# Kernel tuning notes

Hardware: AMD Instinct MI355X
Metric: run time of the kernel (lower is better)

Reference implementation:

```python
import jax, jax.numpy as jnp
import numpy as np
from jax import lax

B = 16384
N_NUM = 32
N_CAT = 16
D = 256
D_HID = 512
N_LAYERS = 8
VOCAB = 100001  # total_cats + 1
OUT_DIM = 2
TOT_FEAT = N_NUM + N_CAT
EPS = 1e-5


def _layernorm(x, g, b):
    mu = jnp.mean(x, axis=-1, keepdims=True)
    var = jnp.mean(jnp.square(x - mu), axis=-1, keepdims=True)
    return (x - mu) * lax.rsqrt(var + EPS) * g + b


def setup_inputs() -> dict:
    key = jax.random.key(0)
    ks = jax.random.split(key, 16)
    s = 0.02
    return {
        "x_numerical": jax.random.normal(ks[0], (B, N_NUM, 1), dtype=jnp.float32),
        "x_categorical_idx": jax.random.randint(ks[1], (B, N_CAT), 0, VOCAB - 1, dtype=jnp.int32),
        # per-feature Linear(1, D): weight [N_NUM, D], bias [N_NUM, D]
        "w_num": jax.random.normal(ks[2], (N_NUM, D), dtype=jnp.float32) * s,
        "b_num": jnp.zeros((N_NUM, D), dtype=jnp.float32),
        "cat_embed": jax.random.normal(ks[3], (VOCAB, D), dtype=jnp.float32) * s,
        "W_first": jax.random.normal(ks[4], (TOT_FEAT * D, D), dtype=jnp.float32) * s,
        "b_first": jnp.zeros((D,), dtype=jnp.float32),
        # stacked block params, leading dim = N_LAYERS
        "ln_g": jnp.ones((N_LAYERS, D), dtype=jnp.float32),
        "ln_b": jnp.zeros((N_LAYERS, D), dtype=jnp.float32),
        "W1s": jax.random.normal(ks[5], (N_LAYERS, D, D_HID), dtype=jnp.float32) * s,
        "b1s": jnp.zeros((N_LAYERS, D_HID), dtype=jnp.float32),
        "W2s": jax.random.normal(ks[6], (N_LAYERS, D_HID, D), dtype=jnp.float32) * s,
        "b2s": jnp.zeros((N_LAYERS, D), dtype=jnp.float32),
        "g_f": jnp.ones((D,), dtype=jnp.float32),
        "beta_f": jnp.zeros((D,), dtype=jnp.float32),
        "W_head": jax.random.normal(ks[7], (D, OUT_DIM), dtype=jnp.float32) * s,
        "b_head": jnp.zeros((OUT_DIM,), dtype=jnp.float32),
    }


def reference(x_numerical, x_categorical_idx, w_num, b_num, cat_embed,
              W_first, b_first, ln_g, ln_b, W1s, b1s, W2s, b2s,
              g_f, beta_f, W_head, b_head):
    # numerical embeddings: per-feature Linear(1, D), vectorized over features
    x_val = x_numerical[:, :, 0:1]                       # [B, N_NUM, 1]
    x_n_emb = x_val * w_num[None] + b_num[None]          # [B, N_NUM, D]
    x_c_emb = cat_embed[x_categorical_idx]               # [B, N_CAT, D]
    x = jnp.concatenate([x_n_emb, x_c_emb], axis=1)      # [B, TOT_FEAT, D]
    x = x.reshape(x.shape[0], -1)                        # [B, TOT_FEAT*D]
    x = x @ W_first + b_first                            # [B, D]

    def block(h, params):
        g, bn, W1, b1, W2, b2 = params
        out = _layernorm(h, g, bn)
        out = jax.nn.relu(out @ W1 + b1)                 # dropout = identity (eval)
        out = out @ W2 + b2
        return h + out, None

    x, _ = lax.scan(block, x, (ln_g, ln_b, W1s, b1s, W2s, b2s))
    x = _layernorm(x, g_f, beta_f)
    logits = x @ W_head + b_head                         # [B, OUT_DIM]
    return logits
```

## Files before the change

### kernel.cpp

```cpp
#include <hip/hip_runtime.h>

typedef unsigned short u16;
typedef unsigned int u32;
typedef __attribute__((ext_vector_type(8))) short bf16x8;
typedef __attribute__((ext_vector_type(4))) float f32x4;

#define LDK 72

__device__ __forceinline__ u16 f2bf(float f) {
    u32 u = __float_as_uint(f);
    u += 0x7fffu + ((u >> 16) & 1u);
    return (u16)(u >> 16);
}

__device__ __forceinline__ f32x4 mfma16(bf16x8 a, bf16x8 b, f32x4 c) {
    return __builtin_amdgcn_mfma_f32_16x16x32_bf16(a, b, c, 0, 0, 0);
}


__global__ __launch_bounds__(256) void prep_u_kernel(
    const float* __restrict__ w_num, const float* __restrict__ b_num,
    const float* __restrict__ W_first, float* __restrict__ U, float* __restrict__ P)
{
    __shared__ float wrow[256];
    __shared__ float brow[256];
    int j = threadIdx.x, f = blockIdx.x;
    wrow[j] = w_num[f * 256 + j];
    brow[j] = b_num[f * 256 + j];
    __syncthreads();
    float au = 0.f, ap = 0.f;
#pragma unroll 8
    for (int k = 0; k < 256; k++) {
        float w = W_first[(size_t)((f << 8) + k) * 256 + j];
        au = fmaf(wrow[k], w, au);
        ap = fmaf(brow[k], w, ap);
    }
    U[f * 256 + j] = au;
    P[f * 256 + j] = ap;
}

__global__ __launch_bounds__(256) void prep_c0_kernel(
    const float* __restrict__ b_first, const float* __restrict__ P, float* __restrict__ c0)
{
    int j = threadIdx.x;
    float a = b_first[j];
#pragma unroll 8
    for (int f = 0; f < 32; f++) a += P[f * 256 + j];
    c0[j] = a;
}

__global__ __launch_bounds__(256) void transpose_kernel(
    const float* __restrict__ in, u16* __restrict__ out,
    int R, int C, int ldo, int k_off, size_t in_stride, size_t out_stride)
{
    __shared__ float t[64][65];
    in  += (size_t)blockIdx.z * in_stride;
    out += (size_t)blockIdx.z * out_stride;
    const int tid = threadIdx.x;
    const int r0 = blockIdx.x * 64, c0 = blockIdx.y * 64;
#pragma unroll
    for (int i = 0; i < 16; i++) {
        int e = tid + i * 256;
        int r = e >> 6, c = e & 63;
        float v = (r0 + r < R) ? in[(size_t)(r0 + r) * C + c0 + c] : 0.f;
        t[c][r] = v;
    }
    __syncthreads();
#pragma unroll
    for (int i = 0; i < 2; i++) {
        int e = tid + i * 256;
        int c = e >> 3, r8 = (e & 7) * 8;
        u16 tmp[8];
#pragma unroll
        for (int x = 0; x < 8; x++) tmp[x] = f2bf(t[c][r8 + x]);
        *(bf16x8*)&out[(size_t)(c0 + c) * ldo + k_off + r0 + r8] = *(bf16x8*)tmp;
    }
}

#define FBM 64

#define GATHER(KQ, G0, G1)                                                    \
    {                                                                         \
        int chunk = tid;                                                      \
        int r = chunk >> 4, c4 = chunk & 15;                                  \
        int k = (KQ) + c4 * 4;                                                \
        int rowi = (k < 4096) ? sidx[r * 16 + ((k >> 8) & 15)] : 0;           \
        G0 = *(const float4*)&cemb[(size_t)rowi * 256 + (k & 255)];           \
        if (k >= 4096) {                                                      \
            if (k < 4128) {                                                   \
                int c = r * 32 + (k - 4096);                                  \
                G0.x = sx[c]; G0.y = sx[c + 1];                               \
                G0.z = sx[c + 2]; G0.w = sx[c + 3];                           \
            } else G0 = make_float4(0.f, 0.f, 0.f, 0.f);                      \
        }                                                                     \
        chunk = tid + 512;                                                    \
        r = chunk >> 4; c4 = chunk & 15;                                      \
        k = (KQ) + c4 * 4;                                                    \
        rowi = (k < 4096) ? sidx[r * 16 + ((k >> 8) & 15)] : 0;               \
        G1 = *(const float4*)&cemb[(size_t)rowi * 256 + (k & 255)];           \
        if (k >= 4096) {                                                      \
            if (k < 4128) {                                                   \
                int c = r * 32 + (k - 4096);                                  \
                G1.x = sx[c]; G1.y = sx[c + 1];                               \
                G1.z = sx[c + 2]; G1.w = sx[c + 3];                           \
            } else G1 = make_float4(0.f, 0.f, 0.f, 0.f);                      \
        }                                                                     \
    }

#define WRITE_A(BUF, G0, G1)                                                  \
    {                                                                         \
        int chunk = tid;                                                      \
        int r = chunk >> 4, c4 = chunk & 15;                                  \
        ushort4 o;                                                            \
        o.x = f2bf(G0.x); o.y = f2bf(G0.y); o.z = f2bf(G0.z); o.w = f2bf(G0.w); \
        *(ushort4*)&Ab[BUF][r * LDK + c4 * 4] = o;                            \
        chunk = tid + 512;                                                    \
        r = chunk >> 4; c4 = chunk & 15;                                      \
        o.x = f2bf(G1.x); o.y = f2bf(G1.y); o.z = f2bf(G1.z); o.w = f2bf(G1.w); \
        *(ushort4*)&Ab[BUF][r * LDK + c4 * 4] = o;                            \
    }

#define DMA_B(BUF, KQ)                                                        \
    _Pragma("unroll")                                                         \
    for (int it = 0; it < 4; it++) {                                          \
        int chunk = it * 512 + tid;                                           \
        int r = chunk >> 3;                                                   \
        int c8 = (chunk & 7) ^ (r & 7);                                       \
        const u16* src = &BT[(size_t)r * 4160 + (KQ) + c8 * 8];               \
        __builtin_amdgcn_global_load_lds(                                     \
            (const __attribute__((address_space(1))) void*)src,               \
            (__attribute__((address_space(3))) void*)&Bb[BUF][(it * 512 + wv * 64) * 8], \
            16, 0, 0);                                                        \
    }

#define COMPUTE(AB, BB)                                                       \
    _Pragma("unroll")                                                         \
    for (int kk = 0; kk < 64; kk += 32) {                                     \
        bf16x8 af[2], bfr[4];                                                 \
        _Pragma("unroll")                                                     \
        for (int i = 0; i < 2; i++)                                           \
            af[i] = *(const bf16x8*)&Ab[AB][(wm * 32 + i * 16 + l16) * LDK + kk + quad * 8]; \
        _Pragma("unroll")                                                     \
        for (int j = 0; j < 4; j++) {                                         \
            int row = wn * 64 + j * 16 + l16;                                 \
            int c8L = quad + (kk >> 3);                                       \
            bfr[j] = *(const bf16x8*)&Bb[BB][row * 64 + ((c8L ^ (row & 7)) * 8)]; \
        }                                                                     \
        _Pragma("unroll")                                                     \
        for (int i = 0; i < 2; i++)                                           \
            _Pragma("unroll")                                                 \
            for (int j = 0; j < 4; j++)                                       \
                acc[i][j] = mfma16(af[i], bfr[j], acc[i][j]);                 \
    }

#define ITER(S, KQ, G0, G1)                                                   \
    {                                                                         \
        WRITE_A((S + 1) & 1, G0, G1);                                         \
        int kq2 = (KQ) + 128; if (kq2 > 4096) kq2 = 4096;                     \
        DMA_B((S + 2) & 3, kq2);                                              \
        __builtin_amdgcn_sched_barrier(0);                                    \
        GATHER((KQ) + 192, G0, G1);                                           \
        __builtin_amdgcn_sched_barrier(0);                                    \
        COMPUTE(S & 1, S);                                                    \
        asm volatile("s_waitcnt vmcnt(8) lgkmcnt(0)" ::: "memory");           \
        __builtin_amdgcn_s_barrier();                                         \
        __builtin_amdgcn_sched_barrier(0);                                    \
    }

__global__ __launch_bounds__(512, 2) void first_gemm_kernel(
    const u16* __restrict__ BT, const float* __restrict__ bias,
    float* __restrict__ outF,
    const int* __restrict__ cidx, const float* __restrict__ cemb,
    const float* __restrict__ xnum)
{
    __shared__ __align__(16) u16 Ab[2][FBM * LDK];
    __shared__ __align__(16) u16 Bb[4][256 * 64];
    __shared__ int   sidx[FBM * 16];
    __shared__ float sx[FBM * 32];

    const int tid  = threadIdx.x;
    const int lane = tid & 63;
    const int wv   = tid >> 6;
    const int wm   = wv >> 2;
    const int wn   = wv & 3;
    const int quad = lane >> 4;
    const int l16  = lane & 15;
    const int m0   = blockIdx.x * FBM;

    sidx[tid]       = cidx[m0 * 16 + tid];
    sidx[tid + 512] = cidx[m0 * 16 + tid + 512];
    {
        float4 v = *(const float4*)&xnum[(size_t)m0 * 32 + tid * 4];
        *(float4*)&sx[tid * 4] = v;
    }
    __syncthreads();

    f32x4 acc[2][4];
#pragma unroll
    for (int i = 0; i < 2; i++)
#pragma unroll
        for (int j = 0; j < 4; j++) acc[i][j] = (f32x4){0.f, 0.f, 0.f, 0.f};

    float4 ga0, ga1, pa0, pa1, pb0, pb1;

    GATHER(0, ga0, ga1);
    WRITE_A(0, ga0, ga1);
    DMA_B(0, 0);
    __builtin_amdgcn_sched_barrier(0);
    GATHER(64, pa0, pa1);
    __builtin_amdgcn_sched_barrier(0);
    DMA_B(1, 64);
    __builtin_amdgcn_sched_barrier(0);
    GATHER(128, pb0, pb1);
    __builtin_amdgcn_sched_barrier(0);
    asm volatile("s_waitcnt vmcnt(8) lgkmcnt(0)" ::: "memory");
    __builtin_amdgcn_s_barrier();
    __builtin_amdgcn_sched_barrier(0);

#pragma unroll 1
    for (int k0 = 0; k0 < 4096; k0 += 256) {
        ITER(0, k0 +   0, pa0, pa1);
        ITER(1, k0 +  64, pb0, pb1);
        ITER(2, k0 + 128, pa0, pa1);
        ITER(3, k0 + 192, pb0, pb1);
    }
    COMPUTE(0, 0);

#pragma unroll
    for (int i = 0; i < 2; i++) {
#pragma unroll
        for (int j = 0; j < 4; j++) {
            int col = wn * 64 + j * 16 + l16;
            float bs = bias[col];
#pragma unroll
            for (int r = 0; r < 4; r++) {
                int row = m0 + wm * 32 + i * 16 + quad * 4 + r;
                outF[(size_t)row * 256 + col] = acc[i][j][r] + bs;
            }
        }
    }
}

__global__ __launch_bounds__(512, 2) void stack_kernel(
    const float* __restrict__ h,
    const float* __restrict__ ln_g, const float* __restrict__ ln_b,
    const u16* __restrict__ W1T, const float* __restrict__ b1s,
    const u16* __restrict__ W2T, const float* __restrict__ b2s,
    const float* __restrict__ g_f, const float* __restrict__ beta_f,
    const float* __restrict__ Wh, const float* __restrict__ bh,
    float* __restrict__ out)
{
    __shared__ __align__(16) float hbuf[64 * 260];
    __shared__ __align__(16) u16   scratch[64 * 520];
    const int tid  = threadIdx.x;
    const int lane = tid & 63;
    const int wv   = tid >> 6;
    const int quad = lane >> 4;
    const int l16  = lane & 15;
    const int m0   = blockIdx.x * 64;

#pragma unroll
    for (int rr = 0; rr < 8; rr++) {
        int row = rr * 8 + wv;
        *(float4*)&hbuf[row * 260 + lane * 4] =
            *(const float4*)&h[(size_t)(m0 + row) * 256 + lane * 4];
    }
    __syncthreads();

#pragma unroll 1
    for (int l = 0; l < 8; l++) {
        const u16* W1 = W1T + l * 131072;
        const u16* W2 = W2T + l * 131072;
        const float* bb1 = b1s + l * 512;
        const float* bb2 = b2s + l * 256;

        float4 gv4 = *(const float4*)&ln_g[l * 256 + lane * 4];
        float4 bv4 = *(const float4*)&ln_b[l * 256 + lane * 4];
#pragma unroll
        for (int rr = 0; rr < 8; rr++) {
            int row = rr * 8 + wv;
            float4 x = *(const float4*)&hbuf[row * 260 + lane * 4];
            float s  = x.x + x.y + x.z + x.w;
            float s2 = x.x * x.x + x.y * x.y + x.z * x.z + x.w * x.w;
#pragma unroll
            for (int o = 32; o > 0; o >>= 1) { s += __shfl_xor(s, o); s2 += __shfl_xor(s2, o); }
            float mu = s * (1.f / 256.f);
            float rs = rsqrtf(s2 * (1.f / 256.f) - mu * mu + 1e-5f);
            ushort4 o4;
            o4.x = f2bf((x.x - mu) * rs * gv4.x + bv4.x);
            o4.y = f2bf((x.y - mu) * rs * gv4.y + bv4.y);
            o4.z = f2bf((x.z - mu) * rs * gv4.z + bv4.z);
            o4.w = f2bf((x.w - mu) * rs * gv4.w + bv4.w);
            *(ushort4*)&scratch[row * 264 + lane * 4] = o4;
        }
        __syncthreads();

        float b1v[4];
#pragma unroll
        for (int j = 0; j < 4; j++) b1v[j] = bb1[wv * 64 + j * 16 + l16];
        f32x4 acc1[4][4];
#pragma unroll
        for (int i = 0; i < 4; i++)
#pragma unroll
            for (int j = 0; j < 4; j++) acc1[i][j] = (f32x4){0.f, 0.f, 0.f, 0.f};
#pragma unroll
        for (int kk = 0; kk < 256; kk += 32) {
            bf16x8 af[4], bw[4];
#pragma unroll
            for (int i = 0; i < 4; i++)
                af[i] = *(const bf16x8*)&scratch[(i * 16 + l16) * 264 + kk + quad * 8];
#pragma unroll
            for (int j = 0; j < 4; j++)
                bw[j] = *(const bf16x8*)&W1[(size_t)(wv * 64 + j * 16 + l16) * 256 + kk + quad * 8];
#pragma unroll
            for (int i = 0; i < 4; i++)
#pragma unroll
                for (int j = 0; j < 4; j++)
                    acc1[i][j] = mfma16(af[i], bw[j], acc1[i][j]);
        }
        __syncthreads();

#pragma unroll
        for (int i = 0; i < 4; i++)
#pragma unroll
            for (int j = 0; j < 4; j++)
#pragma unroll
                for (int r = 0; r < 4; r++) {
                    float v = acc1[i][j][r] + b1v[j];
                    v = v > 0.f ? v : 0.f;
                    scratch[(i * 16 + quad * 4 + r) * 520 + wv * 64 + j * 16 + l16] = f2bf(v);
                }
        __syncthreads();

        float b2v[2];
#pragma unroll
        for (int j = 0; j < 2; j++) b2v[j] = bb2[wv * 32 + j * 16 + l16];
        f32x4 acc2[4][2];
#pragma unroll
        for (int i = 0; i < 4; i++)
#pragma unroll
            for (int j = 0; j < 2; j++) acc2[i][j] = (f32x4){0.f, 0.f, 0.f, 0.f};
#pragma unroll
        for (int kk = 0; kk < 512; kk += 32) {
            bf16x8 af[4], bw[2];
#pragma unroll
            for (int i = 0; i < 4; i++)
                af[i] = *(const bf16x8*)&scratch[(i * 16 + l16) * 520 + kk + quad * 8];
#pragma unroll
            for (int j = 0; j < 2; j++)
                bw[j] = *(const bf16x8*)&W2[(size_t)(wv * 32 + j * 16 + l16) * 512 + kk + quad * 8];
#pragma unroll
            for (int i = 0; i < 4; i++)
#pragma unroll
                for (int j = 0; j < 2; j++)
                    acc2[i][j] = mfma16(af[i], bw[j], acc2[i][j]);
        }

#pragma unroll
        for (int i = 0; i < 4; i++)
#pragma unroll
            for (int j = 0; j < 2; j++) {
                int col = wv * 32 + j * 16 + l16;
#pragma unroll
                for (int r = 0; r < 4; r++)
                    hbuf[(i * 16 + quad * 4 + r) * 260 + col] += acc2[i][j][r] + b2v[j];
            }
        __syncthreads();
    }

    {
        float4 gv4 = *(const float4*)&g_f[lane * 4];
        float4 bv4 = *(const float4*)&beta_f[lane * 4];
        float4 wa = *(const float4*)&Wh[lane * 8];
        float4 wb = *(const float4*)&Wh[lane * 8 + 4];
        float bh0 = bh[0], bh1 = bh[1];
#pragma unroll
        for (int rr = 0; rr < 8; rr++) {
            int row = rr * 8 + wv;
            float4 x = *(const float4*)&hbuf[row * 260 + lane * 4];
            float s = x.x + x.y + x.z + x.w;
            float s2 = x.x * x.x + x.y * x.y + x.z * x.z + x.w * x.w;
#pragma unroll
            for (int o = 32; o > 0; o >>= 1) { s += __shfl_xor(s, o); s2 += __shfl_xor(s2, o); }
            float mu = s * (1.f / 256.f);
            float rs = rsqrtf(s2 * (1.f / 256.f) - mu * mu + 1e-5f);
            float xn0 = (x.x - mu) * rs * gv4.x + bv4.x;
            float xn1 = (x.y - mu) * rs * gv4.y + bv4.y;
            float xn2 = (x.z - mu) * rs * gv4.z + bv4.z;
            float xn3 = (x.w - mu) * rs * gv4.w + bv4.w;
            float d0 = xn0 * wa.x + xn1 * wa.z + xn2 * wb.x + xn3 * wb.z;
            float d1 = xn0 * wa.y + xn1 * wa.w + xn2 * wb.y + xn3 * wb.w;
#pragma unroll
            for (int o = 32; o > 0; o >>= 1) { d0 += __shfl_xor(d0, o); d1 += __shfl_xor(d1, o); }
            if (lane == 0) {
                out[(size_t)(m0 + row) * 2 + 0] = d0 + bh0;
                out[(size_t)(m0 + row) * 2 + 1] = d1 + bh1;
            }
        }
    }
}

extern "C" void kernel_launch(void* const* d_in, const int* in_sizes, int n_in,
                              void* d_out, int out_size, void* d_ws, size_t ws_size,
                              hipStream_t stream)
{
    const float* x_num   = (const float*)d_in[0];
    const int*   cidx    = (const int*)d_in[1];
    const float* w_num   = (const float*)d_in[2];
    const float* b_num   = (const float*)d_in[3];
    const float* cemb    = (const float*)d_in[4];
    const float* W_first = (const float*)d_in[5];
    const float* b_first = (const float*)d_in[6];
    const float* ln_g    = (const float*)d_in[7];
    const float* ln_b    = (const float*)d_in[8];
    const float* W1s     = (const float*)d_in[9];
    const float* b1s     = (const float*)d_in[10];
    const float* W2s     = (const float*)d_in[11];
    const float* b2s     = (const float*)d_in[12];
    const float* g_f     = (const float*)d_in[13];
    const float* beta_f  = (const float*)d_in[14];
    const float* W_head  = (const float*)d_in[15];
    const float* b_head  = (const float*)d_in[16];
    float* out = (float*)d_out;

    char* ws = (char*)d_ws;
    float* U   = (float*)(ws + 0);
    float* c0  = (float*)(ws + 32768);
    float* P   = (float*)(ws + 33792);
    u16* WcT   = (u16*)(ws + 66560);
    u16* W1T   = (u16*)(ws + 2196480);
    u16* W2T   = (u16*)(ws + 4293632);
    float* h   = (float*)(ws + 6390784);

    prep_u_kernel<<<32, 256, 0, stream>>>(w_num, b_num, W_first, U, P);
    prep_c0_kernel<<<1, 256, 0, stream>>>(b_first, P, c0);
    transpose_kernel<<<dim3(64, 4, 1), 256, 0, stream>>>(
        W_first + (size_t)8192 * 256, WcT, 4096, 256, 4160, 0, 0, 0);
    transpose_kernel<<<dim3(1, 4, 1), 256, 0, stream>>>(
        U, WcT, 32, 256, 4160, 4096, 0, 0);
    transpose_kernel<<<dim3(4, 8, 8), 256, 0, stream>>>(
        W1s, W1T, 256, 512, 256, 0, 131072, 131072);
    transpose_kernel<<<dim3(8, 4, 8), 256, 0, stream>>>(
        W2s, W2T, 512, 256, 512, 0, 131072, 131072);

    first_gemm_kernel<<<256, 512, 0, stream>>>(
        WcT, c0, h, cidx, cemb, x_num);

    stack_kernel<<<256, 512, 0, stream>>>(
        h, ln_g, ln_b, W1T, b1s, W2T, b2s,
        g_f, beta_f, W_head, b_head, out);
}
```

Baseline: 458.4 us.

## Prefetch per-layer MLP weights into registers, swizzle LDS, split prep reduction

The stack kernel now preloads each wave's W1 and W2 fragments into registers (32 bf16x8 each) one phase ahead. W2 is loaded during the relu writeback and the next layer's W1 during the residual update, so global weight latency is hidden behind compute. The LDS activation scratch drops its padding in favour of an XOR swizzle to avoid bank conflicts, and barriers become explicit waitcnt plus s_barrier with sched_barriers. The prep_u kernel is split over K into 256 blocks followed by a small reduction kernel, which raises parallelism but adds a launch. The 64 extra vector registers per lane of preloaded weights risk spilling or lower occupancy under launch_bounds(512,2).

```diff
diff --git a/kernel.cpp b/kernel.cpp
--- a/kernel.cpp
+++ b/kernel.cpp
@@ -20,20 +20,37 @@
 
 __global__ __launch_bounds__(256) void prep_u_kernel(
     const float* __restrict__ w_num, const float* __restrict__ b_num,
-    const float* __restrict__ W_first, float* __restrict__ U, float* __restrict__ P)
-{
-    __shared__ float wrow[256];
-    __shared__ float brow[256];
-    int j = threadIdx.x, f = blockIdx.x;
-    wrow[j] = w_num[f * 256 + j];
-    brow[j] = b_num[f * 256 + j];
+    const float* __restrict__ W_first, float* __restrict__ Upart, float* __restrict__ Ppart)
+{
+    __shared__ float wrow[32];
+    __shared__ float brow[32];
+    int j = threadIdx.x, f = blockIdx.x, ks = blockIdx.y;
+    if (j < 32) {
+        wrow[j] = w_num[f * 256 + ks * 32 + j];
+        brow[j] = b_num[f * 256 + ks * 32 + j];
+    }
     __syncthreads();
     float au = 0.f, ap = 0.f;
 #pragma unroll 8
-    for (int k = 0; k < 256; k++) {
-        float w = W_first[(size_t)((f << 8) + k) * 256 + j];
+    for (int k = 0; k < 32; k++) {
+        float w = W_first[(size_t)((f << 8) + ks * 32 + k) * 256 + j];
         au = fmaf(wrow[k], w, au);
         ap = fmaf(brow[k], w, ap);
+    }
+    Upart[(size_t)(ks * 32 + f) * 256 + j] = au;
+    Ppart[(size_t)(ks * 32 + f) * 256 + j] = ap;
+}
+
+__global__ __launch_bounds__(256) void prep_reduce_kernel(
+    const float* __restrict__ Upart, const float* __restrict__ Ppart,
+    float* __restrict__ U, float* __restrict__ P)
+{
+    int j = threadIdx.x, f = blockIdx.x;
+    float au = 0.f, ap = 0.f;
+#pragma unroll
+    for (int ks = 0; ks < 8; ks++) {
+        au += Upart[(size_t)(ks * 32 + f) * 256 + j];
+        ap += Ppart[(size_t)(ks * 32 + f) * 256 + j];
     }
     U[f * 256 + j] = au;
     P[f * 256 + j] = ap;
@@ -241,6 +258,27 @@
     }
 }
 
+#define BAR()                                                                 \
+    asm volatile("s_waitcnt lgkmcnt(0)" ::: "memory");                        \
+    __builtin_amdgcn_s_barrier();                                             \
+    __builtin_amdgcn_sched_barrier(0);
+
+#define PRELOAD_W1(LIDX)                                                      \
+    __builtin_amdgcn_sched_barrier(0);                                        \
+    _Pragma("unroll")                                                         \
+    for (int s = 0; s < 32; s++)                                              \
+        w1r[s] = *(const bf16x8*)&W1T[(size_t)(LIDX) * 131072 +               \
+            (size_t)(wv * 64 + (s & 3) * 16 + l16) * 256 + (s >> 2) * 32 + quad * 8]; \
+    __builtin_amdgcn_sched_barrier(0);
+
+#define PRELOAD_W2(LIDX)                                                      \
+    __builtin_amdgcn_sched_barrier(0);                                        \
+    _Pragma("unroll")                                                         \
+    for (int s = 0; s < 32; s++)                                              \
+        w2r[s] = *(const bf16x8*)&W2T[(size_t)(LIDX) * 131072 +               \
+            (size_t)(wv * 32 + (s & 1) * 16 + l16) * 512 + (s >> 1) * 32 + quad * 8]; \
+    __builtin_amdgcn_sched_barrier(0);
+
 __global__ __launch_bounds__(512, 2) void stack_kernel(
     const float* __restrict__ h,
     const float* __restrict__ ln_g, const float* __restrict__ ln_b,
@@ -251,7 +289,7 @@
     float* __restrict__ out)
 {
     __shared__ __align__(16) float hbuf[64 * 260];
-    __shared__ __align__(16) u16   scratch[64 * 520];
+    __shared__ __align__(16) u16   scratch[64 * 512];
     const int tid  = threadIdx.x;
     const int lane = tid & 63;
     const int wv   = tid >> 6;
@@ -259,18 +297,20 @@
     const int l16  = lane & 15;
     const int m0   = blockIdx.x * 64;
 
+    bf16x8 w1r[32], w2r[32];
+
+    PRELOAD_W1(0)
+
 #pragma unroll
     for (int rr = 0; rr < 8; rr++) {
         int row = rr * 8 + wv;
         *(float4*)&hbuf[row * 260 + lane * 4] =
             *(const float4*)&h[(size_t)(m0 + row) * 256 + lane * 4];
     }
-    __syncthreads();
+    BAR();
 
 #pragma unroll 1
     for (int l = 0; l < 8; l++) {
-        const u16* W1 = W1T + l * 131072;
-        const u16* W2 = W2T + l * 131072;
         const float* bb1 = b1s + l * 512;
         const float* bb2 = b2s + l * 256;
 
@@ -291,9 +331,9 @@
             o4.y = f2bf((x.y - mu) * rs * gv4.y + bv4.y);
             o4.z = f2bf((x.z - mu) * rs * gv4.z + bv4.z);
             o4.w = f2bf((x.w - mu) * rs * gv4.w + bv4.w);
-            *(ushort4*)&scratch[row * 264 + lane * 4] = o4;
-        }
-        __syncthreads();
+            *(ushort4*)&scratch[row * 256 + (((lane >> 1) ^ (row & 7)) << 3) + (lane & 1) * 4] = o4;
+        }
+        BAR();
 
         float b1v[4];
 #pragma unroll
@@ -304,21 +344,21 @@
 #pragma unroll
             for (int j = 0; j < 4; j++) acc1[i][j] = (f32x4){0.f, 0.f, 0.f, 0.f};
 #pragma unroll
-        for (int kk = 0; kk < 256; kk += 32) {
-            bf16x8 af[4], bw[4];
+        for (int ks = 0; ks < 8; ks++) {
+            bf16x8 af[4];
 #pragma unroll
             for (int i = 0; i < 4; i++)
-                af[i] = *(const bf16x8*)&scratch[(i * 16 + l16) * 264 + kk + quad * 8];
-#pragma unroll
-            for (int j = 0; j < 4; j++)
-                bw[j] = *(const bf16x8*)&W1[(size_t)(wv * 64 + j * 16 + l16) * 256 + kk + quad * 8];
+                af[i] = *(const bf16x8*)&scratch[(i * 16 + l16) * 256 +
+                            (((ks * 4 + quad) ^ (l16 & 7)) << 3)];
 #pragma unroll
             for (int i = 0; i < 4; i++)
 #pragma unroll
                 for (int j = 0; j < 4; j++)
-                    acc1[i][j] = mfma16(af[i], bw[j], acc1[i][j]);
-        }
-        __syncthreads();
+                    acc1[i][j] = mfma16(af[i], w1r[ks * 4 + j], acc1[i][j]);
+        }
+
+        PRELOAD_W2(l)
+        BAR();
 
 #pragma unroll
         for (int i = 0; i < 4; i++)
@@ -328,9 +368,11 @@
                 for (int r = 0; r < 4; r++) {
                     float v = acc1[i][j][r] + b1v[j];
                     v = v > 0.f ? v : 0.f;
-                    scratch[(i * 16 + quad * 4 + r) * 520 + wv * 64 + j * 16 + l16] = f2bf(v);
+                    int row2 = i * 16 + quad * 4 + r;
+                    int col  = wv * 64 + j * 16 + l16;
+                    scratch[row2 * 512 + (((col >> 3) ^ (row2 & 7)) << 3) + (col & 7)] = f2bf(v);
                 }
-        __syncthreads();
+        BAR();
 
         float b2v[2];
 #pragma unroll
@@ -341,19 +383,21 @@
 #pragma unroll
             for (int j = 0; j < 2; j++) acc2[i][j] = (f32x4){0.f, 0.f, 0.f, 0.f};
 #pragma unroll
-        for (int kk = 0; kk < 512; kk += 32) {
-            bf16x8 af[4], bw[2];
+        for (int ks = 0; ks < 16; ks++) {
+            bf16x8 af[4];
 #pragma unroll
             for (int i = 0; i < 4; i++)
-                af[i] = *(const bf16x8*)&scratch[(i * 16 + l16) * 520 + kk + quad * 8];
-#pragma unroll
-            for (int j = 0; j < 2; j++)
-                bw[j] = *(const bf16x8*)&W2[(size_t)(wv * 32 + j * 16 + l16) * 512 + kk + quad * 8];
+                af[i] = *(const bf16x8*)&scratch[(i * 16 + l16) * 512 +
+                            (((ks * 4 + quad) ^ (l16 & 7)) << 3)];
 #pragma unroll
             for (int i = 0; i < 4; i++)
 #pragma unroll
                 for (int j = 0; j < 2; j++)
-                    acc2[i][j] = mfma16(af[i], bw[j], acc2[i][j]);
+                    acc2[i][j] = mfma16(af[i], w2r[ks * 2 + j], acc2[i][j]);
+        }
+
+        if (l < 7) {
+            PRELOAD_W1(l + 1)
         }
 
 #pragma unroll
@@ -365,7 +409,7 @@
                 for (int r = 0; r < 4; r++)
                     hbuf[(i * 16 + quad * 4 + r) * 260 + col] += acc2[i][j][r] + b2v[j];
             }
-        __syncthreads();
+        BAR();
     }
 
     {
@@ -431,8 +475,11 @@
     u16* W1T   = (u16*)(ws + 2196480);
     u16* W2T   = (u16*)(ws + 4293632);
     float* h   = (float*)(ws + 6390784);
-
-    prep_u_kernel<<<32, 256, 0, stream>>>(w_num, b_num, W_first, U, P);
+    float* Upart = (float*)(ws + 2196480);
+    float* Ppart = (float*)(ws + 2458624);
+
+    prep_u_kernel<<<dim3(32, 8), 256, 0, stream>>>(w_num, b_num, W_first, Upart, Ppart);
+    prep_reduce_kernel<<<32, 256, 0, stream>>>(Upart, Ppart, U, P);
     prep_c0_kernel<<<1, 256, 0, stream>>>(b_first, P, c0);
     transpose_kernel<<<dim3(64, 4, 1), 256, 0, stream>>>(
         W_first + (size_t)8192 * 256, WcT, 4096, 256, 4160, 0, 0, 0);
```

New measurement: 766.3 us. 1.67x slower.
